# Performance work log

Hardware: AMD Instinct MI355X
Metric: run time of the kernel (lower is better)

Reference implementation:

```python
import jax, jax.numpy as jnp
import numpy as np

NW = 4096      # num_words in document
H = 768        # encoder hidden size
NC = 49152     # number of candidate spans
MSW = 30       # max_span_width
E = 20         # span width embedding size
M = 1024       # mlp hidden size
SPAN_EMB = 3 * H + E  # ment_emb='attn' -> start + end + attn term + width emb
NEG = -1e10


def setup_inputs() -> dict:
    key = jax.random.key(0)
    ks = jax.random.split(key, 16)
    s = 0.02
    encoded_doc = jax.random.normal(ks[0], (NW, H), jnp.float32)
    cand_starts = jax.random.randint(ks[1], (NC,), 0, NW - MSW)
    widths = jax.random.randint(ks[2], (NC,), 0, MSW)
    cand_ends = cand_starts + widths  # guaranteed < NW
    return {
        "encoded_doc": encoded_doc,
        "cand_starts": cand_starts,
        "cand_ends": cand_ends,
        "width_emb": jax.random.normal(ks[3], (MSW, E), jnp.float32) * s,
        "width_prior_emb": jax.random.normal(ks[4], (MSW, E), jnp.float32) * s,
        "attn_w": jax.random.normal(ks[5], (H,), jnp.float32) * s,
        "attn_b": jnp.zeros((1,), jnp.float32),
        "mlp1_w": jax.random.normal(ks[6], (SPAN_EMB, M), jnp.float32) * s,
        "mlp1_b": jnp.zeros((M,), jnp.float32),
        "mlp2_w": jax.random.normal(ks[7], (M,), jnp.float32) * s,
        "mlp2_b": jnp.zeros((1,), jnp.float32),
        "wmlp1_w": jax.random.normal(ks[8], (E, M), jnp.float32) * s,
        "wmlp1_b": jnp.zeros((M,), jnp.float32),
        "wmlp2_w": jax.random.normal(ks[9], (M,), jnp.float32) * s,
        "wmlp2_b": jnp.zeros((1,), jnp.float32),
    }


def reference(encoded_doc, cand_starts, cand_ends, width_emb, width_prior_emb,
              attn_w, attn_b, mlp1_w, mlp1_b, mlp2_w, mlp2_b,
              wmlp1_w, wmlp1_b, wmlp2_w, wmlp2_b):
    # span width index (clamped), shared by both width embedding tables
    width_idx = jnp.clip(cand_ends - cand_starts, 0, MSW - 1)

    # --- get_span_embeddings ---
    start_emb = encoded_doc[cand_starts]                 # [NC, H]
    end_emb = encoded_doc[cand_ends]                     # [NC, H]
    w_emb = width_emb[width_idx]                         # [NC, E]

    word_attn = encoded_doc @ attn_w + attn_b[0]         # [NW]
    doc_range = jnp.arange(NW)
    ment_mask = (doc_range[None, :] >= cand_starts[:, None]) & \
                (doc_range[None, :] <= cand_ends[:, None])       # [NC, NW]
    # original: (1 - mask)*-1e10 + word_attn
    scores = jnp.where(ment_mask, 0.0, NEG) + word_attn[None, :]
    mention_word_attn = jax.nn.softmax(scores, axis=1)   # [NC, NW]
    attention_term = mention_word_attn @ encoded_doc     # [NC, H]

    span_emb = jnp.concatenate([start_emb, end_emb, w_emb, attention_term],
                               axis=1)                   # [NC, 3H+E]

    # --- mention_mlp scoring (1 hidden ReLU layer -> scalar) ---
    h = jax.nn.relu(span_emb @ mlp1_w + mlp1_b)          # [NC, M]
    mention_logits = h @ mlp2_w + mlp2_b[0]              # [NC]

    # --- get_mention_width_scores ---
    wp = width_prior_emb[width_idx]                      # [NC, E]
    hw = jax.nn.relu(wp @ wmlp1_w + wmlp1_b)             # [NC, M]
    width_scores = hw @ wmlp2_w + wmlp2_b[0]             # [NC]

    return mention_logits + width_scores
```

## Files before the change

kernel.cpp:

```cpp
#include <hip/hip_runtime.h>
#include <math.h>

#define NW 4096
#define H 768
#define NC 49152
#define MSW 30
#define E 20
#define M 1024
#define CHUNK 64
#define NCH (NW / CHUNK)
#define NKT (H / 64)

typedef short bf16x8 __attribute__((ext_vector_type(8)));
typedef unsigned short u16x8 __attribute__((ext_vector_type(8)));
typedef float f32x4 __attribute__((ext_vector_type(4)));

__device__ __forceinline__ unsigned short f2bf(float x) {
    unsigned u = __float_as_uint(x);
    return (unsigned short)((u + 0x7fff + ((u >> 16) & 1)) >> 16);
}
__device__ __forceinline__ float bf2f(unsigned short b) {
    return __uint_as_float(((unsigned)b) << 16);
}
__device__ __forceinline__ void gload16(const void* g, void* l) {
    __builtin_amdgcn_global_load_lds((const __attribute__((address_space(1))) void*)g,
                                     (__attribute__((address_space(3))) void*)l, 16, 0, 0);
}

__global__ __launch_bounds__(256) void k_prep(const float* __restrict__ doc,
                                              const float* __restrict__ attn_w,
                                              const float* __restrict__ attn_b,
                                              unsigned short* __restrict__ docb,
                                              float* __restrict__ ewa,
                                              int* __restrict__ hist,
                                              const float* __restrict__ mlp1_w,
                                              unsigned short* __restrict__ Bt,
                                              const float* __restrict__ width_emb,
                                              const float* __restrict__ mlp1_b,
                                              float* __restrict__ PW,
                                              const float* __restrict__ wp_emb,
                                              const float* __restrict__ w1,
                                              const float* __restrict__ b1,
                                              const float* __restrict__ w2,
                                              const float* __restrict__ b2,
                                              float* __restrict__ wscore) {
    __shared__ float sh[32][33];
    __shared__ float red[256];
    int bx = blockIdx.x;
    int tid = threadIdx.x;
    if (bx < 1024) {
        if (bx < 16) hist[bx * 256 + tid] = 0;
        int row = bx * 4 + (tid >> 6);
        int lane = tid & 63;
        const float* r = doc + (size_t)row * H;
        float s = 0.f;
        #pragma unroll
        for (int q = 0; q < 3; ++q) {
            int idx = q * 256 + lane * 4;
            float4 v = *reinterpret_cast<const float4*>(r + idx);
            float4 w = *reinterpret_cast<const float4*>(attn_w + idx);
            s += v.x * w.x + v.y * w.y + v.z * w.z + v.w * w.w;
            ushort4 o;
            o.x = f2bf(v.x); o.y = f2bf(v.y); o.z = f2bf(v.z); o.w = f2bf(v.w);
            *reinterpret_cast<ushort4*>(docb + (size_t)row * H + idx) = o;
        }
        #pragma unroll
        for (int off = 32; off > 0; off >>= 1) s += __shfl_down(s, off);
        if (lane == 0) ewa[row] = expf(s + attn_b[0]);
    } else if (bx < 3328) {
        int idx = bx - 1024;
        int k0 = (idx % 24) * 32;
        int m0 = ((idx / 24) % 32) * 32;
        int part = idx / (24 * 32);
        int rb = part == 0 ? 0 : (part == 1 ? H : (2 * H + E));
        int tx = tid & 31, ty = tid >> 5;
        #pragma unroll
        for (int it = 0; it < 4; ++it) {
            int kk = ty + it * 8;
            sh[kk][tx] = mlp1_w[(size_t)(rb + k0 + kk) * M + m0 + tx];
        }
        __syncthreads();
        #pragma unroll
        for (int it = 0; it < 4; ++it) {
            int mm = ty + it * 8;
            Bt[(size_t)(part * M + m0 + mm) * H + k0 + tx] = f2bf(sh[tx][mm]);
        }
    } else {
        int idx = bx - 3328;
        int w = idx / 5, y = idx % 5;
        if (y < 4) {
            int m = y * 256 + tid;
            float acc = mlp1_b[m];
            #pragma unroll
            for (int e = 0; e < E; ++e)
                acc += width_emb[w * E + e] * mlp1_w[(size_t)(2 * H + e) * M + m];
            PW[w * M + m] = acc;
        } else {
            float part = 0.f;
            for (int m = tid; m < M; m += 256) {
                float h = b1[m];
                #pragma unroll
                for (int e = 0; e < E; ++e) h += wp_emb[w * E + e] * w1[e * M + m];
                part += fmaxf(h, 0.f) * w2[m];
            }
            red[tid] = part;
            __syncthreads();
            for (int s = 128; s > 0; s >>= 1) {
                if (tid < s) red[tid] += red[tid + s];
                __syncthreads();
            }
            if (tid == 0) wscore[w] = red[0] + b2[0];
        }
    }
}

__global__ __launch_bounds__(256) void k_scans2(const float* __restrict__ ewa,
                                                float* __restrict__ Dpre,
                                                const int* __restrict__ hist,
                                                int* __restrict__ offs,
                                                int* __restrict__ begs) {
    __shared__ float shf[256];
    __shared__ int shi[256];
    int t = threadIdx.x;
    if (blockIdx.x == 0) {
        float v[16];
        float sum = 0.f;
        #pragma unroll
        for (int i = 0; i < 16; ++i) { v[i] = ewa[t * 16 + i]; sum += v[i]; }
        shf[t] = sum;
        __syncthreads();
        for (int off = 1; off < 256; off <<= 1) {
            float x = (t >= off) ? shf[t - off] : 0.f;
            __syncthreads();
            shf[t] += x;
            __syncthreads();
        }
        float run = shf[t] - sum;
        #pragma unroll
        for (int i = 0; i < 16; ++i) { run += v[i]; Dpre[t * 16 + i + 1] = run; }
        if (t == 0) Dpre[0] = 0.f;
    } else {
        int v[16];
        int sum = 0;
        #pragma unroll
        for (int i = 0; i < 16; ++i) { v[i] = hist[t * 16 + i]; sum += v[i]; }
        shi[t] = sum;
        __syncthreads();
        for (int off = 1; off < 256; off <<= 1) {
            int x = (t >= off) ? shi[t - off] : 0;
            __syncthreads();
            shi[t] += x;
            __syncthreads();
        }
        int run = shi[t] - sum;
        #pragma unroll
        for (int i = 0; i < 16; ++i) {
            offs[t * 16 + i] = run;
            begs[t * 16 + i] = run;
            run += v[i];
        }
        if (t == 255) begs[4096] = run;
    }
}

__global__ __launch_bounds__(256) void k_hist(const int* __restrict__ starts,
                                              int* __restrict__ hist) {
    atomicAdd(&hist[starts[blockIdx.x * 256 + threadIdx.x]], 1);
}
__global__ __launch_bounds__(256) void k_scatter(const int* __restrict__ starts,
                                                 int* __restrict__ offs,
                                                 int* __restrict__ perm) {
    int c = blockIdx.x * 256 + threadIdx.x;
    int p = atomicAdd(&offs[starts[c]], 1);
    perm[p] = c;
}

__global__ __launch_bounds__(512, 4) void k_proj_mfma(const unsigned short* __restrict__ docb,
                                                      const unsigned short* __restrict__ Bt,
                                                      const float* __restrict__ ewa,
                                                      unsigned short* __restrict__ Pse,
                                                      float* __restrict__ Sbuf,
                                                      float* __restrict__ T) {
    __shared__ unsigned short As[2][8192];
    __shared__ unsigned short Bs[2][12288];
    int tid = threadIdx.x;
    int bid = blockIdx.x;
    int xcd = bid & 7, rr0 = bid >> 3;
    int coltile = (xcd & 1) * 8 + (rr0 & 7);
    int rowtile = (xcd >> 1) * 8 + (rr0 >> 3);
    int col0 = coltile * 192;
    int row0 = rowtile * 128;
    int wv = tid >> 6, lane = tid & 63;
    int wr = wv >> 2, wc = wv & 3;

    f32x4 acc[4][3];
    #pragma unroll
    for (int mi = 0; mi < 4; ++mi)
        #pragma unroll
        for (int ni = 0; ni < 3; ++ni) acc[mi][ni] = (f32x4){0.f, 0.f, 0.f, 0.f};

    #define STAGE(buf, k0)                                                            \
        {                                                                             \
            _Pragma("unroll")                                                         \
            for (int i = 0; i < 2; ++i) {                                             \
                int s = i * 512 + tid;                                                \
                int mg = s >> 7, ks = (s >> 6) & 1, g = (s >> 4) & 3, ri = s & 15;    \
                gload16(docb + (size_t)(row0 + mg * 16 + ri) * H + (k0) + ks * 32 + g * 8, \
                        (char*)As[buf] + s * 16);                                     \
            }                                                                         \
            _Pragma("unroll")                                                         \
            for (int i = 0; i < 3; ++i) {                                             \
                int s = i * 512 + tid;                                                \
                int cg = s >> 7, ks = (s >> 6) & 1, g = (s >> 4) & 3, ci = s & 15;    \
                gload16(Bt + (size_t)(col0 + cg * 16 + ci) * H + (k0) + ks * 32 + g * 8, \
                        (char*)Bs[buf] + s * 16);                                     \
            }                                                                         \
        }

    STAGE(0, 0);
    STAGE(1, 64);
    asm volatile("s_waitcnt vmcnt(5)" ::: "memory");
    __builtin_amdgcn_s_barrier();

    #pragma unroll 1
    for (int t = 0; t < NKT; ++t) {
        int cur = t & 1;
        #pragma unroll
        for (int ks = 0; ks < 2; ++ks) {
            bf16x8 af[4], bfr[3];
            #pragma unroll
            for (int mi = 0; mi < 4; ++mi)
                af[mi] = *reinterpret_cast<const bf16x8*>(
                    (char*)As[cur] + (wr * 4 + mi) * 2048 + ks * 1024 + lane * 16);
            #pragma unroll
            for (int ni = 0; ni < 3; ++ni)
                bfr[ni] = *reinterpret_cast<const bf16x8*>(
                    (char*)Bs[cur] + (wc * 3 + ni) * 2048 + ks * 1024 + lane * 16);
            __builtin_amdgcn_s_setprio(1);
            #pragma unroll
            for (int mi = 0; mi < 4; ++mi)
                #pragma unroll
                for (int ni = 0; ni < 3; ++ni)
                    acc[mi][ni] = __builtin_amdgcn_mfma_f32_16x16x32_bf16(
                        af[mi], bfr[ni], acc[mi][ni], 0, 0, 0);
            __builtin_amdgcn_s_setprio(0);
        }
        if (t + 2 < NKT) {
            asm volatile("s_waitcnt lgkmcnt(0)" ::: "memory");
            __builtin_amdgcn_sched_barrier(0);
            __builtin_amdgcn_s_barrier();
            STAGE(cur, (t + 2) * 64);
            asm volatile("s_waitcnt vmcnt(5)" ::: "memory");
            __builtin_amdgcn_s_barrier();
        } else if (t + 2 == NKT) {
            asm volatile("s_waitcnt vmcnt(0)" ::: "memory");
            __builtin_amdgcn_s_barrier();
        }
    }
    #undef STAGE

    int cr = (lane >> 4) * 4;
    int cc = lane & 15;
    #pragma unroll
    for (int mi = 0; mi < 4; ++mi) {
        #pragma unroll
        for (int ni = 0; ni < 3; ++ni) {
            int rrow = row0 + wr * 64 + mi * 16 + cr;
            int cabs = col0 + wc * 48 + ni * 16 + cc;
            int part = cabs >> 10;
            int cm = cabs & 1023;
            if (part < 2) {
                unsigned short* dst = Pse + (size_t)rrow * 2048 + part * 1024 + cm;
                #pragma unroll
                for (int j = 0; j < 4; ++j) dst[(size_t)j * 2048] = f2bf(acc[mi][ni][j]);
            } else {
                float* dst = Sbuf + (size_t)rrow * M + cm;
                #pragma unroll
                for (int j = 0; j < 4; ++j) dst[(size_t)j * M] = acc[mi][ni][j];
            }
        }
    }
    {
        int chunk = (row0 >> 6) + wr;
        #pragma unroll
        for (int ni = 0; ni < 3; ++ni) {
            int cabs = col0 + wc * 48 + ni * 16 + cc;
            if (cabs >= 2048) {
                float psum = 0.f;
                #pragma unroll
                for (int mi = 0; mi < 4; ++mi) {
                    int rbase = row0 + wr * 64 + mi * 16 + cr;
                    #pragma unroll
                    for (int j = 0; j < 4; ++j)
                        psum += ewa[rbase + j] * acc[mi][ni][j];
                }
                psum += __shfl_down(psum, 16);
                psum += __shfl_down(psum, 32);
                if ((lane >> 4) == 0)
                    T[(size_t)chunk * M + (cabs - 2048)] = psum;
            }
        }
    }
}

__global__ __launch_bounds__(256) void k_scan3(float* __restrict__ Sbuf,
                                               const float* __restrict__ ewa,
                                               const float* __restrict__ T) {
    int m = blockIdx.x * 256 + threadIdx.x;
    int c = blockIdx.y;
    __shared__ float ew[CHUNK];
    if (threadIdx.x < CHUNK) ew[threadIdx.x] = ewa[c * CHUNK + threadIdx.x];
    __syncthreads();
    float acc = 0.f;
    for (int cp = 0; cp < c; ++cp) acc += T[(size_t)cp * M + m];
    float* base = Sbuf + (size_t)(c * CHUNK) * M + m;
    #pragma unroll 4
    for (int i = 0; i < CHUNK; ++i) {
        float* p = base + (size_t)i * M;
        acc += ew[i] * (*p);
        *p = acc;
    }
}

__global__ __launch_bounds__(256) void k_cand(const unsigned short* __restrict__ Pse,
                                              const float* __restrict__ Sbuf,
                                              const float* __restrict__ PW,
                                              const float* __restrict__ Dpre,
                                              const float* __restrict__ wscore,
                                              const int* __restrict__ perm,
                                              const int* __restrict__ begs,
                                              const int* __restrict__ ends,
                                              const float* __restrict__ mlp2_w,
                                              const float* __restrict__ mlp2_b,
                                              float* __restrict__ out) {
    __shared__ __align__(16) unsigned short ps_l[1024];
    __shared__ __align__(16) float ss_l[1024];
    int bid = blockIdx.x;
    int s = (bid & 7) * 512 + (bid >> 3);
    int tid = threadIdx.x;
    {
        ushort4 p4 = *reinterpret_cast<const ushort4*>(Pse + (size_t)s * 2048 + tid * 4);
        *reinterpret_cast<ushort4*>(ps_l + tid * 4) = p4;
        float4 s4 = (s > 0) ? *reinterpret_cast<const float4*>(Sbuf + (size_t)(s - 1) * M + tid * 4)
                            : make_float4(0.f, 0.f, 0.f, 0.f);
        *reinterpret_cast<float4*>(ss_l + tid * 4) = s4;
    }
    __syncthreads();
    int beg = begs[s], end = begs[s + 1];
    int wv = tid >> 6, lane = tid & 63;
    float dps = Dpre[s];
    float4 v00 = *reinterpret_cast<const float4*>(mlp2_w + lane * 8);
    float4 v01 = *reinterpret_cast<const float4*>(mlp2_w + lane * 8 + 4);
    float4 v10 = *reinterpret_cast<const float4*>(mlp2_w + lane * 8 + 512);
    float4 v11 = *reinterpret_cast<const float4*>(mlp2_w + lane * 8 + 516);

    for (int j = beg + wv; j < end; j += 4) {
        int c = perm[j];
        int e = ends[c];
        int wi = e - s;
        wi = wi > MSW - 1 ? MSW - 1 : wi;
        float inv = 1.f / (Dpre[e + 1] - dps);
        const unsigned short* pe = Pse + (size_t)e * 2048 + 1024;
        const float* se = Sbuf + (size_t)e * M;
        const float* pw = PW + (size_t)wi * M;

        float part = 0.f;
        #pragma unroll
        for (int q = 0; q < 2; ++q) {
            int m = lane * 8 + q * 512;
            u16x8 a8 = *reinterpret_cast<const u16x8*>(ps_l + m);
            u16x8 b8 = *reinterpret_cast<const u16x8*>(pe + m);
            float4 t0 = *reinterpret_cast<const float4*>(se + m);
            float4 t1 = *reinterpret_cast<const float4*>(se + m + 4);
            float4 u0 = *reinterpret_cast<const float4*>(ss_l + m);
            float4 u1 = *reinterpret_cast<const float4*>(ss_l + m + 4);
            float4 w0 = *reinterpret_cast<const float4*>(pw + m);
            float4 w1 = *reinterpret_cast<const float4*>(pw + m + 4);
            float4 v0 = q ? v10 : v00;
            float4 v1 = q ? v11 : v01;
            float x;
            x = bf2f(a8[0]) + bf2f(b8[0]) + w0.x + (t0.x - u0.x) * inv; part += fmaxf(x, 0.f) * v0.x;
            x = bf2f(a8[1]) + bf2f(b8[1]) + w0.y + (t0.y - u0.y) * inv; part += fmaxf(x, 0.f) * v0.y;
            x = bf2f(a8[2]) + bf2f(b8[2]) + w0.z + (t0.z - u0.z) * inv; part += fmaxf(x, 0.f) * v0.z;
            x = bf2f(a8[3]) + bf2f(b8[3]) + w0.w + (t0.w - u0.w) * inv; part += fmaxf(x, 0.f) * v0.w;
            x = bf2f(a8[4]) + bf2f(b8[4]) + w1.x + (t1.x - u1.x) * inv; part += fmaxf(x, 0.f) * v1.x;
            x = bf2f(a8[5]) + bf2f(b8[5]) + w1.y + (t1.y - u1.y) * inv; part += fmaxf(x, 0.f) * v1.y;
            x = bf2f(a8[6]) + bf2f(b8[6]) + w1.z + (t1.z - u1.z) * inv; part += fmaxf(x, 0.f) * v1.z;
            x = bf2f(a8[7]) + bf2f(b8[7]) + w1.w + (t1.w - u1.w) * inv; part += fmaxf(x, 0.f) * v1.w;
        }
        #pragma unroll
        for (int off = 32; off > 0; off >>= 1) part += __shfl_down(part, off);
        if (lane == 0) out[c] = part + mlp2_b[0] + wscore[wi];
    }
}

extern "C" void kernel_launch(void* const* d_in, const int* in_sizes, int n_in,
                              void* d_out, int out_size, void* d_ws, size_t ws_size,
                              hipStream_t stream) {
    const float* encoded_doc = (const float*)d_in[0];
    const int*   cand_starts = (const int*)d_in[1];
    const int*   cand_ends   = (const int*)d_in[2];
    const float* width_emb   = (const float*)d_in[3];
    const float* width_prior = (const float*)d_in[4];
    const float* attn_w      = (const float*)d_in[5];
    const float* attn_b      = (const float*)d_in[6];
    const float* mlp1_w      = (const float*)d_in[7];
    const float* mlp1_b      = (const float*)d_in[8];
    const float* mlp2_w      = (const float*)d_in[9];
    const float* mlp2_b      = (const float*)d_in[10];
    const float* wmlp1_w     = (const float*)d_in[11];
    const float* wmlp1_b     = (const float*)d_in[12];
    const float* wmlp2_w     = (const float*)d_in[13];
    const float* wmlp2_b     = (const float*)d_in[14];
    float* out = (float*)d_out;

    float* Sbuf   = (float*)d_ws;
    float* T      = Sbuf + (size_t)NW * M;
    float* PW     = T + NCH * M;
    float* ewa    = PW + MSW * M;
    float* Dpre   = ewa + NW;
    float* wscore = Dpre + 4160;
    unsigned short* Pse  = (unsigned short*)(wscore + 64);
    unsigned short* docb = Pse + (size_t)NW * 2048;
    unsigned short* Btb  = docb + (size_t)NW * H;
    int* hist = (int*)(Btb + (size_t)3072 * H);
    int* offs = hist + 4096;
    int* begs = offs + 4096;
    int* perm = begs + 4112;

    k_prep<<<3478, 256, 0, stream>>>(encoded_doc, attn_w, attn_b, docb, ewa, hist,
                                     mlp1_w, Btb, width_emb, mlp1_b, PW,
                                     width_prior, wmlp1_w, wmlp1_b, wmlp2_w, wmlp2_b, wscore);
    k_hist<<<NC / 256, 256, 0, stream>>>(cand_starts, hist);
    k_scans2<<<2, 256, 0, stream>>>(ewa, Dpre, hist, offs, begs);
    k_scatter<<<NC / 256, 256, 0, stream>>>(cand_starts, offs, perm);
    k_proj_mfma<<<512, 512, 0, stream>>>(docb, Btb, ewa, Pse, Sbuf, T);
    k_scan3<<<dim3(M / 256, NCH), 256, 0, stream>>>(Sbuf, ewa, T);
    k_cand<<<4096, 256, 0, stream>>>(Pse, Sbuf, PW, Dpre, wscore, perm, begs,
                                     cand_ends, mlp2_w, mlp2_b, out);
}
```

Baseline: 119.4 us.

## Drop LDS staging in projection GEMM and load MFMA fragments directly from global

The projection GEMM no longer stages A and B tiles through double-buffered shared memory with global_load_lds and barriers. Each of four waves now loads its bf16 fragments straight from global memory, and per-wave tiles grow from 4x3 to 4x6 MFMA tiles, so blocks use 256 threads instead of 512. This removes LDS traffic and barrier synchronisation. In exchange it loses cross-wave data reuse, adds L2 traffic, and raises register pressure with 24 accumulators and fully unrolled K loops.

```diff
diff --git a/kernel.cpp b/kernel.cpp
--- a/kernel.cpp
+++ b/kernel.cpp
@@ -21,10 +21,6 @@
 }
 __device__ __forceinline__ float bf2f(unsigned short b) {
     return __uint_as_float(((unsigned)b) << 16);
-}
-__device__ __forceinline__ void gload16(const void* g, void* l) {
-    __builtin_amdgcn_global_load_lds((const __attribute__((address_space(1))) void*)g,
-                                     (__attribute__((address_space(3))) void*)l, 16, 0, 0);
 }
 
 __global__ __launch_bounds__(256) void k_prep(const float* __restrict__ doc,
@@ -175,14 +171,12 @@
     perm[p] = c;
 }
 
-__global__ __launch_bounds__(512, 4) void k_proj_mfma(const unsigned short* __restrict__ docb,
+__global__ __launch_bounds__(256, 2) void k_proj_mfma(const unsigned short* __restrict__ docb,
                                                       const unsigned short* __restrict__ Bt,
                                                       const float* __restrict__ ewa,
                                                       unsigned short* __restrict__ Pse,
                                                       float* __restrict__ Sbuf,
                                                       float* __restrict__ T) {
-    __shared__ unsigned short As[2][8192];
-    __shared__ unsigned short Bs[2][12288];
     int tid = threadIdx.x;
     int bid = blockIdx.x;
     int xcd = bid & 7, rr0 = bid >> 3;
@@ -191,82 +185,47 @@
     int col0 = coltile * 192;
     int row0 = rowtile * 128;
     int wv = tid >> 6, lane = tid & 63;
-    int wr = wv >> 2, wc = wv & 3;
-
-    f32x4 acc[4][3];
+    int wr = wv >> 1, wc = wv & 1;
+    int fr = lane & 15, kq = lane >> 4;
+
+    const unsigned short* Abase = docb + (size_t)(row0 + wr * 64 + fr) * H + kq * 8;
+    const unsigned short* Bbase = Bt + (size_t)(col0 + wc * 96 + fr) * H + kq * 8;
+
+    f32x4 acc[4][6];
     #pragma unroll
     for (int mi = 0; mi < 4; ++mi)
         #pragma unroll
-        for (int ni = 0; ni < 3; ++ni) acc[mi][ni] = (f32x4){0.f, 0.f, 0.f, 0.f};
-
-    #define STAGE(buf, k0)                                                            \
-        {                                                                             \
-            _Pragma("unroll")                                                         \
-            for (int i = 0; i < 2; ++i) {                                             \
-                int s = i * 512 + tid;                                                \
-                int mg = s >> 7, ks = (s >> 6) & 1, g = (s >> 4) & 3, ri = s & 15;    \
-                gload16(docb + (size_t)(row0 + mg * 16 + ri) * H + (k0) + ks * 32 + g * 8, \
-                        (char*)As[buf] + s * 16);                                     \
-            }                                                                         \
-            _Pragma("unroll")                                                         \
-            for (int i = 0; i < 3; ++i) {                                             \
-                int s = i * 512 + tid;                                                \
-                int cg = s >> 7, ks = (s >> 6) & 1, g = (s >> 4) & 3, ci = s & 15;    \
-                gload16(Bt + (size_t)(col0 + cg * 16 + ci) * H + (k0) + ks * 32 + g * 8, \
-                        (char*)Bs[buf] + s * 16);                                     \
-            }                                                                         \
-        }
-
-    STAGE(0, 0);
-    STAGE(1, 64);
-    asm volatile("s_waitcnt vmcnt(5)" ::: "memory");
-    __builtin_amdgcn_s_barrier();
-
-    #pragma unroll 1
+        for (int ni = 0; ni < 6; ++ni) acc[mi][ni] = (f32x4){0.f, 0.f, 0.f, 0.f};
+
+    #pragma unroll
     for (int t = 0; t < NKT; ++t) {
-        int cur = t & 1;
         #pragma unroll
         for (int ks = 0; ks < 2; ++ks) {
-            bf16x8 af[4], bfr[3];
+            int ko = t * 64 + ks * 32;
+            bf16x8 af[4], bfr[6];
             #pragma unroll
             for (int mi = 0; mi < 4; ++mi)
-                af[mi] = *reinterpret_cast<const bf16x8*>(
-                    (char*)As[cur] + (wr * 4 + mi) * 2048 + ks * 1024 + lane * 16);
+                af[mi] = *reinterpret_cast<const bf16x8*>(Abase + (size_t)mi * 16 * H + ko);
             #pragma unroll
-            for (int ni = 0; ni < 3; ++ni)
-                bfr[ni] = *reinterpret_cast<const bf16x8*>(
-                    (char*)Bs[cur] + (wc * 3 + ni) * 2048 + ks * 1024 + lane * 16);
-            __builtin_amdgcn_s_setprio(1);
+            for (int ni = 0; ni < 6; ++ni)
+                bfr[ni] = *reinterpret_cast<const bf16x8*>(Bbase + (size_t)ni * 16 * H + ko);
             #pragma unroll
             for (int mi = 0; mi < 4; ++mi)
                 #pragma unroll
-                for (int ni = 0; ni < 3; ++ni)
+                for (int ni = 0; ni < 6; ++ni)
                     acc[mi][ni] = __builtin_amdgcn_mfma_f32_16x16x32_bf16(
                         af[mi], bfr[ni], acc[mi][ni], 0, 0, 0);
-            __builtin_amdgcn_s_setprio(0);
-        }
-        if (t + 2 < NKT) {
-            asm volatile("s_waitcnt lgkmcnt(0)" ::: "memory");
-            __builtin_amdgcn_sched_barrier(0);
-            __builtin_amdgcn_s_barrier();
-            STAGE(cur, (t + 2) * 64);
-            asm volatile("s_waitcnt vmcnt(5)" ::: "memory");
-            __builtin_amdgcn_s_barrier();
-        } else if (t + 2 == NKT) {
-            asm volatile("s_waitcnt vmcnt(0)" ::: "memory");
-            __builtin_amdgcn_s_barrier();
-        }
-    }
-    #undef STAGE
+        }
+    }
 
     int cr = (lane >> 4) * 4;
     int cc = lane & 15;
     #pragma unroll
     for (int mi = 0; mi < 4; ++mi) {
         #pragma unroll
-        for (int ni = 0; ni < 3; ++ni) {
+        for (int ni = 0; ni < 6; ++ni) {
             int rrow = row0 + wr * 64 + mi * 16 + cr;
-            int cabs = col0 + wc * 48 + ni * 16 + cc;
+            int cabs = col0 + wc * 96 + ni * 16 + cc;
             int part = cabs >> 10;
             int cm = cabs & 1023;
             if (part < 2) {
@@ -283,8 +242,8 @@
     {
         int chunk = (row0 >> 6) + wr;
         #pragma unroll
-        for (int ni = 0; ni < 3; ++ni) {
-            int cabs = col0 + wc * 48 + ni * 16 + cc;
+        for (int ni = 0; ni < 6; ++ni) {
+            int cabs = col0 + wc * 96 + ni * 16 + cc;
             if (cabs >= 2048) {
                 float psum = 0.f;
                 #pragma unroll
@@ -434,7 +393,7 @@
     k_hist<<<NC / 256, 256, 0, stream>>>(cand_starts, hist);
     k_scans2<<<2, 256, 0, stream>>>(ewa, Dpre, hist, offs, begs);
     k_scatter<<<NC / 256, 256, 0, stream>>>(cand_starts, offs, perm);
-    k_proj_mfma<<<512, 512, 0, stream>>>(docb, Btb, ewa, Pse, Sbuf, T);
+    k_proj_mfma<<<512, 256, 0, stream>>>(docb, Btb, ewa, Pse, Sbuf, T);
     k_scan3<<<dim3(M / 256, NCH), 256, 0, stream>>>(Sbuf, ewa, T);
     k_cand<<<4096, 256, 0, stream>>>(Pse, Sbuf, PW, Dpre, wscore, perm, begs,
                                      cand_ends, mlp2_w, mlp2_b, out);
```

After: 145.3 us. 21.7% more time.
